# Kernel tuning notes

Measured on AMD Instinct MI355X. Metric: run time of the kernel, lower is better.

The kernel has to match this reference:

```python
import jax, jax.numpy as jnp
import numpy as np
import math

L, B, D, H = 2048, 4, 1024, 16
DK = D // H
DFF = 4 * D
EPS = 1e-5


def setup_inputs() -> dict:
    key = jax.random.key(0)
    ks = jax.random.split(key, 16)
    s = 1.0 / math.sqrt(D)
    sf = 1.0 / math.sqrt(DFF)
    return {
        "x": jax.random.normal(ks[0], (L, B, D), jnp.float32),
        "Wq": jax.random.normal(ks[1], (D, D), jnp.float32) * s,
        "bq": jnp.zeros((D,), jnp.float32),
        "Wk": jax.random.normal(ks[2], (D, D), jnp.float32) * s,
        "bk": jnp.zeros((D,), jnp.float32),
        "Wv": jax.random.normal(ks[3], (D, D), jnp.float32) * s,
        "bv": jnp.zeros((D,), jnp.float32),
        "Wo": jax.random.normal(ks[4], (D, D), jnp.float32) * s,
        "bo": jnp.zeros((D,), jnp.float32),
        "W1": jax.random.normal(ks[5], (D, DFF), jnp.float32) * s,
        "b1": jnp.zeros((DFF,), jnp.float32),
        "W2": jax.random.normal(ks[6], (DFF, D), jnp.float32) * sf,
        "b2": jnp.zeros((D,), jnp.float32),
        "g1": jnp.ones((D,), jnp.float32),
        "be1": jnp.zeros((D,), jnp.float32),
        "g2": jnp.ones((D,), jnp.float32),
        "be2": jnp.zeros((D,), jnp.float32),
    }


def _layer_norm(x, g, b):
    mu = jnp.mean(x, axis=-1, keepdims=True)
    var = jnp.var(x, axis=-1, keepdims=True)
    return (x - mu) * jax.lax.rsqrt(var + EPS) * g + b


def reference(x, Wq, bq, Wk, bk, Wv, bv, Wo, bo, W1, b1, W2, b2, g1, be1, g2, be2):
    # x: (L, B, D)
    q = x @ Wq + bq
    k = x @ Wk + bk
    v = x @ Wv + bv
    # (L,B,H,dk) -> (B,H,L,dk)
    q = q.reshape(L, B, H, DK).transpose(1, 2, 0, 3)
    k = k.reshape(L, B, H, DK).transpose(1, 2, 0, 3)
    v = v.reshape(L, B, H, DK).transpose(1, 2, 0, 3)
    scale = 1.0 / math.sqrt(DK)
    scores = jnp.einsum('bhqd,bhkd->bhqk', q, k) * scale
    w = jax.nn.softmax(scores, axis=-1)
    attn = jnp.einsum('bhqk,bhkd->bhqd', w, v)  # (B,H,L,dk)
    attn = attn.transpose(2, 0, 1, 3).reshape(L, B, D)
    attn_out = attn @ Wo + bo
    x = _layer_norm(x + attn_out, g1, be1)
    h = jax.nn.gelu(x @ W1 + b1, approximate=False)
    ff = h @ W2 + b2
    return _layer_norm(x + ff, g2, be2)
```

## Files before the change

### kernel.cpp

```cpp
#include <hip/hip_runtime.h>

#define L_   2048
#define B_   4
#define D_   1024
#define H_   16
#define DK_  64
#define DFF_ 4096
#define NT_  (L_*B_)

typedef unsigned short u16;
typedef unsigned int   u32;
typedef __bf16 bf16x8 __attribute__((ext_vector_type(8)));
typedef float  f32x4  __attribute__((ext_vector_type(4)));

__device__ __forceinline__ u16 f2bf(float f) {
  u32 u = __float_as_uint(f);
  u += 0x7fffu + ((u >> 16) & 1u);
  return (u16)(u >> 16);
}

#define GLDS16(g, l) __builtin_amdgcn_global_load_lds( \
    (const __attribute__((address_space(1))) void*)(g), \
    (__attribute__((address_space(3))) void*)(l), 16, 0, 0)

__global__ __launch_bounds__(256) void transpose_w_k(
    const float* __restrict__ W, u16* __restrict__ Wt, int K, int N)
{
  __shared__ float tile[32][33];
  int n0 = blockIdx.x * 32, k0 = blockIdx.y * 32;
  int tx = threadIdx.x, ty = threadIdx.y;
#pragma unroll
  for (int i = ty; i < 32; i += 8)
    tile[i][tx] = W[(size_t)(k0 + i) * N + n0 + tx];
  __syncthreads();
#pragma unroll
  for (int i = ty; i < 32; i += 8)
    Wt[(size_t)(n0 + i) * K + k0 + tx] = f2bf(tile[tx][i]);
}

__global__ __launch_bounds__(256) void f32_to_bf16_k(
    const float* __restrict__ in, u16* __restrict__ out, int n4)
{
  int i = blockIdx.x * 256 + threadIdx.x;
  if (i >= n4) return;
  float4 v = ((const float4*)in)[i];
  uint2 r;
  r.x = (u32)f2bf(v.x) | ((u32)f2bf(v.y) << 16);
  r.y = (u32)f2bf(v.z) | ((u32)f2bf(v.w) << 16);
  ((uint2*)out)[i] = r;
}

__global__ __launch_bounds__(256) void bias_concat_k(
    const float* __restrict__ bq, const float* __restrict__ bk,
    const float* __restrict__ bv, float* __restrict__ o)
{
  int i = blockIdx.x * 256 + threadIdx.x;
  float v = (i < 1024) ? bq[i] : ((i < 2048) ? bk[i - 1024] : bv[i - 2048]);
  o[i] = v;
}

template<int BN, int EPI>
__global__ __launch_bounds__(512, 2)
void gemm_pipe(const u16* __restrict__ A, const u16* __restrict__ Bt,
               const float* __restrict__ bias, const float* __restrict__ res,
               u16* __restrict__ outb, float* __restrict__ outf,
               int M, int N, int K)
{
  constexpr int BM = 256;
  constexpr int NI  = 2 + BN / 128;
  constexpr int NWN = BN / 64;
  constexpr int NWM = 8 / NWN;
  constexpr int MIT = (BM / NWM) / 16;
  constexpr int NPH = MIT / 4;
  constexpr int BUFB = (BM + BN) * 64;
  __shared__ char SM[4 * BUFB];

  const int tid = threadIdx.x;
  const int w = tid >> 6, lane = tid & 63;
  const int l15 = lane & 15, l4 = lane >> 4;
  const int NK = K >> 5;

  const int gx = gridDim.x;
  int nwg = gx * gridDim.y;
  int id = blockIdx.y * gx + blockIdx.x;
  int q = nwg >> 3, r = nwg & 7;
  int xcd = id & 7, idx = id >> 3;
  int wg = (xcd < r ? xcd * (q + 1) : r * (q + 1) + (xcd - r) * q) + idx;
  const int m0 = (wg / gx) * BM, n0 = (wg % gx) * BN;
  const int wm = (w / NWN) * (BM / NWM), wn = (w % NWN) * 64;

  const u16* gsrc[NI];
#pragma unroll
  for (int k = 0; k < NI; ++k) {
    int o = k * 8192 + tid * 16;
    int col8 = (o >> 4) & 3;
    if (o < BM * 64) {
      int rrow = o >> 6;
      gsrc[k] = A + (size_t)(m0 + rrow) * K + col8 * 8;
    } else {
      int br = (o - BM * 64) >> 6;
      gsrc[k] = Bt + (size_t)(n0 + br) * K + col8 * 8;
    }
  }

  auto stage = [&](int t3, int k) {
    const u16* s = (t3 < NK) ? gsrc[k] + (size_t)t3 * 32 : gsrc[k];
    GLDS16(s, SM + (t3 & 3) * BUFB + k * 8192 + w * 1024);
  };

  for (int t3 = 0; t3 < 3; ++t3)
#pragma unroll
    for (int k = 0; k < NI; ++k) stage(t3, k);
  if constexpr (BN == 256) asm volatile("s_waitcnt vmcnt(8)" ::: "memory");
  else                     asm volatile("s_waitcnt vmcnt(6)" ::: "memory");
  asm volatile("s_barrier" ::: "memory");

  f32x4 acc[MIT][4];
#pragma unroll
  for (int i = 0; i < MIT; ++i)
#pragma unroll
    for (int j = 0; j < 4; ++j) acc[i][j] = (f32x4){0.f, 0.f, 0.f, 0.f};

  for (int t = 0; t < NK; ++t) {
    const char* rb = SM + (t & 3) * BUFB;
    bf16x8 bfr[4];
#pragma unroll
    for (int ph = 0; ph < NPH; ++ph) {
      bf16x8 af[4];
#pragma unroll
      for (int mi = 0; mi < 4; ++mi)
        af[mi] = *(const bf16x8*)(rb + (wm + ph * 64 + mi * 16 + l15) * 64 + l4 * 16);
      if (ph == 0) {
#pragma unroll
        for (int nj = 0; nj < 4; ++nj)
          bfr[nj] = *(const bf16x8*)(rb + BM * 64 + (wn + nj * 16 + l15) * 64 + l4 * 16);
      }
      if constexpr (NPH == 2) {
        stage(t + 3, ph * 2 + 0);
        stage(t + 3, ph * 2 + 1);
      } else {
        stage(t + 3, 0); stage(t + 3, 1); stage(t + 3, 2);
      }
      asm volatile("s_barrier" ::: "memory");
      __builtin_amdgcn_s_setprio(1);
#pragma unroll
      for (int mi = 0; mi < 4; ++mi)
#pragma unroll
        for (int nj = 0; nj < 4; ++nj)
          acc[ph * 4 + mi][nj] = __builtin_amdgcn_mfma_f32_16x16x32_bf16(
              af[mi], bfr[nj], acc[ph * 4 + mi][nj], 0, 0, 0);
      __builtin_amdgcn_s_setprio(0);
      if (ph == NPH - 1) {
        if constexpr (BN == 256) asm volatile("s_waitcnt vmcnt(8)" ::: "memory");
        else                     asm volatile("s_waitcnt vmcnt(6)" ::: "memory");
      }
      asm volatile("s_barrier" ::: "memory");
    }
  }
  asm volatile("s_waitcnt vmcnt(0)" ::: "memory");

  const int gm = m0 + wm + l4 * 4;
  const int gn = n0 + wn + l15;
#pragma unroll
  for (int mi = 0; mi < MIT; ++mi) {
#pragma unroll
    for (int nj = 0; nj < 4; ++nj) {
      int col = gn + nj * 16;
      float bv = bias[col];
#pragma unroll
      for (int rr = 0; rr < 4; ++rr) {
        int row = gm + mi * 16 + rr;
        float v = acc[mi][nj][rr] + bv;
        if (EPI == 1) {
          size_t idxo = (size_t)row * N + col;
          outf[idxo] = v + res[idxo];
        } else if (EPI == 2) {
          float gv = 0.5f * v * (1.f + erff(v * 0.70710678118654752f));
          outb[(size_t)row * N + col] = f2bf(gv);
        } else {
          int which = col >> 10, c1 = col & 1023;
          int ll = row >> 2, bb = row & 3;
          int hh = c1 >> 6, dd = c1 & 63;
          outb[(size_t)which * (L_ * B_ * D_ / 4) * 4 / 2 * 2 +
               ((((size_t)(bb * H_ + hh)) * L_ + ll) << 6) + dd
               - (size_t)which * 0] = f2bf(v);
        }
      }
    }
  }
}

template<>
__global__ __launch_bounds__(512, 2)
void gemm_pipe<256, 3>(const u16* __restrict__ A, const u16* __restrict__ Bt,
                       const float* __restrict__ bias, const float* __restrict__ res,
                       u16* __restrict__ outb, float* __restrict__ outf,
                       int M, int N, int K)
{
  constexpr int BM = 256, BN = 256;
  constexpr int NI = 4, NWN = 4, NWM = 2, MIT = 8, NPH = 2;
  constexpr int BUFB = (BM + BN) * 64;
  __shared__ char SM[4 * BUFB];

  const int tid = threadIdx.x;
  const int w = tid >> 6, lane = tid & 63;
  const int l15 = lane & 15, l4 = lane >> 4;
  const int NK = K >> 5;

  const int gx = gridDim.x;
  int nwg = gx * gridDim.y;
  int id = blockIdx.y * gx + blockIdx.x;
  int q = nwg >> 3, r = nwg & 7;
  int xcd = id & 7, idx = id >> 3;
  int wg = (xcd < r ? xcd * (q + 1) : r * (q + 1) + (xcd - r) * q) + idx;
  const int m0 = (wg / gx) * BM, n0 = (wg % gx) * BN;
  const int wm = (w / NWN) * (BM / NWM), wn = (w % NWN) * 64;

  const u16* gsrc[NI];
#pragma unroll
  for (int k = 0; k < NI; ++k) {
    int o = k * 8192 + tid * 16;
    int col8 = (o >> 4) & 3;
    if (o < BM * 64) {
      int rrow = o >> 6;
      gsrc[k] = A + (size_t)(m0 + rrow) * K + col8 * 8;
    } else {
      int br = (o - BM * 64) >> 6;
      gsrc[k] = Bt + (size_t)(n0 + br) * K + col8 * 8;
    }
  }

  auto stage = [&](int t3, int k) {
    const u16* s = (t3 < NK) ? gsrc[k] + (size_t)t3 * 32 : gsrc[k];
    GLDS16(s, SM + (t3 & 3) * BUFB + k * 8192 + w * 1024);
  };

  for (int t3 = 0; t3 < 3; ++t3)
#pragma unroll
    for (int k = 0; k < NI; ++k) stage(t3, k);
  asm volatile("s_waitcnt vmcnt(8)" ::: "memory");
  asm volatile("s_barrier" ::: "memory");

  f32x4 acc[MIT][4];
#pragma unroll
  for (int i = 0; i < MIT; ++i)
#pragma unroll
    for (int j = 0; j < 4; ++j) acc[i][j] = (f32x4){0.f, 0.f, 0.f, 0.f};

  for (int t = 0; t < NK; ++t) {
    const char* rb = SM + (t & 3) * BUFB;
    bf16x8 bfr[4];
#pragma unroll
    for (int ph = 0; ph < NPH; ++ph) {
      bf16x8 af[4];
#pragma unroll
      for (int mi = 0; mi < 4; ++mi)
        af[mi] = *(const bf16x8*)(rb + (wm + ph * 64 + mi * 16 + l15) * 64 + l4 * 16);
      if (ph == 0) {
#pragma unroll
        for (int nj = 0; nj < 4; ++nj)
          bfr[nj] = *(const bf16x8*)(rb + BM * 64 + (wn + nj * 16 + l15) * 64 + l4 * 16);
      }
      stage(t + 3, ph * 2 + 0);
      stage(t + 3, ph * 2 + 1);
      asm volatile("s_barrier" ::: "memory");
      __builtin_amdgcn_s_setprio(1);
#pragma unroll
      for (int mi = 0; mi < 4; ++mi)
#pragma unroll
        for (int nj = 0; nj < 4; ++nj)
          acc[ph * 4 + mi][nj] = __builtin_amdgcn_mfma_f32_16x16x32_bf16(
              af[mi], bfr[nj], acc[ph * 4 + mi][nj], 0, 0, 0);
      __builtin_amdgcn_s_setprio(0);
      if (ph == NPH - 1) asm volatile("s_waitcnt vmcnt(8)" ::: "memory");
      asm volatile("s_barrier" ::: "memory");
    }
  }
  asm volatile("s_waitcnt vmcnt(0)" ::: "memory");

  const int gm = m0 + wm + l4 * 4;
  const int gn = n0 + wn + l15;
#pragma unroll
  for (int mi = 0; mi < MIT; ++mi) {
#pragma unroll
    for (int nj = 0; nj < 4; ++nj) {
      int col = gn + nj * 16;
      float bv = bias[col];
#pragma unroll
      for (int rr = 0; rr < 4; ++rr) {
        int row = gm + mi * 16 + rr;
        float v = acc[mi][nj][rr] + bv;
        int which = col >> 10, c1 = col & 1023;
        int ll = row >> 2, bb = row & 3;
        int hh = c1 >> 6, dd = c1 & 63;
        outb[(size_t)which * 8388608 +
             ((((size_t)(bb * H_ + hh)) * L_ + ll) << 6) + dd] = f2bf(v);
      }
    }
  }
}

__global__ __launch_bounds__(256, 4)
void attn_fwd2(const u16* __restrict__ qp, const u16* __restrict__ kp,
               const u16* __restrict__ vp, u16* __restrict__ op)
{
  __shared__ u16 Ks[64 * 64];
  __shared__ u16 Vt[64 * 64];
  const int tid = threadIdx.x, w = tid >> 6, lane = tid & 63;
  const int l15 = lane & 15, l4 = lane >> 4;
  const int n = blockIdx.x;
  const int bh = (n & 7) | ((n >> 8) << 3);
  const int qi = (n >> 3) & 31;
  const int q0 = qi * 64;
  const u16* qb = qp + (size_t)bh * L_ * DK_;
  const u16* kb = kp + (size_t)bh * L_ * DK_;
  const u16* vb = vp + (size_t)bh * L_ * DK_;

  bf16x8 qf[2];
#pragma unroll
  for (int kk = 0; kk < 2; ++kk)
    qf[kk] = *(const bf16x8*)&qb[(size_t)(q0 + w * 16 + l15) * DK_ + kk * 32 + l4 * 8];

  f32x4 accO[4];
#pragma unroll
  for (int i = 0; i < 4; ++i) accO[i] = (f32x4){0.f, 0.f, 0.f, 0.f};
  float mrun = -1e30f, lsum = 0.f;
  const float SC = 0.18033688011112042f;

  int rho0 = tid >> 3, rho1 = (256 + tid) >> 3, c = lane & 7;
  int kv0 = (rho0 & 32) | ((rho0 & 12) << 1) | ((rho0 & 16) >> 2) | (rho0 & 3);
  int kv1 = (rho1 & 32) | ((rho1 & 12) << 1) | ((rho1 & 16) >> 2) | (rho1 & 3);
  const u16* ksrc0 = kb + (size_t)kv0 * DK_ + ((c ^ (rho0 & 7)) << 3);
  const u16* ksrc1 = kb + (size_t)kv1 * DK_ + ((c ^ (rho1 & 7)) << 3);
  u16* kdst0 = &Ks[(w * 64) * 8];
  u16* kdst1 = &Ks[(256 + w * 64) * 8];

  const int vseg = tid & 7, vkvp = tid >> 3;
  const u16* vsrc = vb + (size_t)(vkvp * 2) * DK_ + vseg * 8;
  u32* vdst[8];
#pragma unroll
  for (int dd2 = 0; dd2 < 4; ++dd2) {
    int d0 = vseg * 8 + dd2 * 2, d1 = d0 + 1;
    vdst[dd2 * 2] = (u32*)((char*)Vt + d0 * 128 +
        ((((vkvp >> 2) ^ (d0 & 7) ^ (d0 >> 3)) << 4) | ((vkvp & 3) << 2)));
    vdst[dd2 * 2 + 1] = (u32*)((char*)Vt + d1 * 128 +
        ((((vkvp >> 2) ^ (d1 & 7) ^ (d1 >> 3)) << 4) | ((vkvp & 3) << 2)));
  }

  for (int t0 = 0; t0 < L_; t0 += 64) {
    __syncthreads();
    GLDS16(ksrc0 + (size_t)t0 * DK_, kdst0);
    GLDS16(ksrc1 + (size_t)t0 * DK_, kdst1);
    {
      const u16* src = vsrc + (size_t)t0 * DK_;
      uint4 a = *(const uint4*)src;
      uint4 b = *(const uint4*)(src + DK_);
#pragma unroll
      for (int dd2 = 0; dd2 < 4; ++dd2) {
        u32 ai = ((const u32*)&a)[dd2], bi = ((const u32*)&b)[dd2];
        *vdst[dd2 * 2]     = (ai & 0xFFFFu) | (bi << 16);
        *vdst[dd2 * 2 + 1] = (ai >> 16) | (bi & 0xFFFF0000u);
      }
    }
    __syncthreads();

    f32x4 s[4];
#pragma unroll
    for (int i = 0; i < 4; ++i) s[i] = (f32x4){0.f, 0.f, 0.f, 0.f};
#pragma unroll
    for (int kk = 0; kk < 2; ++kk) {
#pragma unroll
      for (int nb = 0; nb < 4; ++nb) {
        int row = nb * 16 + l15;
        bf16x8 kf = *(const bf16x8*)((const char*)Ks + row * 128 +
                                     (((kk * 4 + l4) ^ (row & 7)) << 4));
        s[nb] = __builtin_amdgcn_mfma_f32_16x16x32_bf16(kf, qf[kk], s[nb], 0, 0, 0);
      }
    }

    float pm = s[0][0];
#pragma unroll
    for (int i = 0; i < 4; ++i)
#pragma unroll
      for (int rr = 0; rr < 4; ++rr) pm = fmaxf(pm, s[i][rr]);
    pm = fmaxf(pm, __shfl_xor(pm, 16));
    pm = fmaxf(pm, __shfl_xor(pm, 32));
    float pmS = pm * SC;
    if (!__all(pmS - mrun <= 8.f)) {
      float mn = fmaxf(mrun, pmS);
      float alpha = exp2f(mrun - mn);
      mrun = mn;
      lsum *= alpha;
#pragma unroll
      for (int rr = 0; rr < 4; ++rr) {
        float a4 = __shfl(alpha, l4 * 4 + rr);
        accO[0][rr] *= a4; accO[1][rr] *= a4; accO[2][rr] *= a4; accO[3][rr] *= a4;
      }
    }
#pragma unroll
    for (int i = 0; i < 4; ++i)
#pragma unroll
      for (int rr = 0; rr < 4; ++rr) s[i][rr] = exp2f(fmaf(s[i][rr], SC, -mrun));
    float ps = 0.f;
#pragma unroll
    for (int i = 0; i < 4; ++i)
      ps += (s[i][0] + s[i][1]) + (s[i][2] + s[i][3]);
    ps += __shfl_xor(ps, 16);
    ps += __shfl_xor(ps, 32);
    lsum += ps;

    u32 pk[2][4];
#pragma unroll
    for (int kk = 0; kk < 2; ++kk)
#pragma unroll
      for (int j2 = 0; j2 < 4; ++j2) {
        int nb = kk * 2 + (j2 >> 1);
        int rr = (j2 & 1) * 2;
        u32 rres;
        asm("v_cvt_pk_bf16_f32 %0, %1, %2" : "=v"(rres) : "v"(s[nb][rr]), "v"(s[nb][rr + 1]));
        pk[kk][j2] = rres;
      }

#pragma unroll
    for (int kk = 0; kk < 2; ++kk) {
      bf16x8 pa;
      ((u32*)&pa)[0] = pk[kk][0];
      ((u32*)&pa)[1] = pk[kk][1];
      ((u32*)&pa)[2] = pk[kk][2];
      ((u32*)&pa)[3] = pk[kk][3];
#pragma unroll
      for (int nb2 = 0; nb2 < 4; ++nb2) {
        int drow = nb2 * 16 + l15;
        bf16x8 vf = *(const bf16x8*)((const char*)Vt + drow * 128 +
                                     (((kk * 4 + l4) ^ (drow & 7) ^ (drow >> 3)) << 4));
        accO[nb2] = __builtin_amdgcn_mfma_f32_16x16x32_bf16(pa, vf, accO[nb2], 0, 0, 0);
      }
    }
  }

  float invl = 1.f / lsum;
  const int bb = bh >> 4, hh = bh & 15;
#pragma unroll
  for (int rr = 0; rr < 4; ++rr) {
    float rl = __shfl(invl, l4 * 4 + rr);
    int qg = q0 + w * 16 + l4 * 4 + rr;
    size_t base = ((size_t)qg * B_ + bb) * D_ + hh * 64;
#pragma unroll
    for (int nb2 = 0; nb2 < 4; ++nb2)
      op[base + nb2 * 16 + l15] = f2bf(accO[nb2][rr] * rl);
  }
}

__global__ __launch_bounds__(256) void layernorm_k(
    const float* __restrict__ y, const float* __restrict__ g, const float* __restrict__ be,
    float* __restrict__ of, u16* __restrict__ ob)
{
  int row = blockIdx.x, tid = threadIdx.x;
  const float4 v = *(const float4*)&y[(size_t)row * D_ + tid * 4];
  float s = v.x + v.y + v.z + v.w;
  float ss = v.x * v.x + v.y * v.y + v.z * v.z + v.w * v.w;
#pragma unroll
  for (int msk = 32; msk >= 1; msk >>= 1) {
    s += __shfl_xor(s, msk);
    ss += __shfl_xor(ss, msk);
  }
  __shared__ float rs[4], rss[4];
  if ((tid & 63) == 0) { rs[tid >> 6] = s; rss[tid >> 6] = ss; }
  __syncthreads();
  s = rs[0] + rs[1] + rs[2] + rs[3];
  ss = rss[0] + rss[1] + rss[2] + rss[3];
  float mu = s * (1.f / D_);
  float var = ss * (1.f / D_) - mu * mu;
  float rstd = rsqrtf(var + 1e-5f);
  int c = tid * 4;
  float4 o;
  o.x = (v.x - mu) * rstd * g[c + 0] + be[c + 0];
  o.y = (v.y - mu) * rstd * g[c + 1] + be[c + 1];
  o.z = (v.z - mu) * rstd * g[c + 2] + be[c + 2];
  o.w = (v.w - mu) * rstd * g[c + 3] + be[c + 3];
  *(float4*)&of[(size_t)row * D_ + c] = o;
  if (ob) {
    uint2 r;
    r.x = (u32)f2bf(o.x) | ((u32)f2bf(o.y) << 16);
    r.y = (u32)f2bf(o.z) | ((u32)f2bf(o.w) << 16);
    *(uint2*)&ob[(size_t)row * D_ + c] = r;
  }
}

extern "C" void kernel_launch(void* const* d_in, const int* in_sizes, int n_in,
                              void* d_out, int out_size, void* d_ws, size_t ws_size,
                              hipStream_t stream)
{
  const float* x   = (const float*)d_in[0];
  const float* Wq  = (const float*)d_in[1];
  const float* bq  = (const float*)d_in[2];
  const float* Wk  = (const float*)d_in[3];
  const float* bk  = (const float*)d_in[4];
  const float* Wv  = (const float*)d_in[5];
  const float* bv  = (const float*)d_in[6];
  const float* Wo  = (const float*)d_in[7];
  const float* bo  = (const float*)d_in[8];
  const float* W1  = (const float*)d_in[9];
  const float* b1  = (const float*)d_in[10];
  const float* W2  = (const float*)d_in[11];
  const float* b2  = (const float*)d_in[12];
  const float* g1  = (const float*)d_in[13];
  const float* be1 = (const float*)d_in[14];
  const float* g2  = (const float*)d_in[15];
  const float* be2 = (const float*)d_in[16];

  char* ws = (char*)d_ws;
  const size_t MB = 1024 * 1024;
  u16* WqT  = (u16*)(ws + 0 * MB);
  u16* WkT  = (u16*)(ws + 2 * MB);
  u16* WvT  = (u16*)(ws + 4 * MB);
  u16* WoT  = (u16*)(ws + 6 * MB);
  u16* W1T  = (u16*)(ws + 8 * MB);
  u16* W2T  = (u16*)(ws + 16 * MB);
  u16* xb   = (u16*)(ws + 24 * MB);
  u16* qp   = (u16*)(ws + 40 * MB);
  u16* astd = (u16*)(ws + 88 * MB);
  float* y1  = (float*)(ws + 104 * MB);
  float* x1f = (float*)(ws + 136 * MB);
  u16*   x1b = (u16*)(ws + 168 * MB);
  float* bcat = (float*)(ws + 184 * MB);
  u16*   hbuf = (u16*)(ws + 40 * MB);
  u16* kp = qp + 8388608;
  u16* vp = qp + 16777216;

  dim3 tb(32, 8);
  transpose_w_k<<<dim3(32, 32), tb, 0, stream>>>(Wq, WqT, D_, D_);
  transpose_w_k<<<dim3(32, 32), tb, 0, stream>>>(Wk, WkT, D_, D_);
  transpose_w_k<<<dim3(32, 32), tb, 0, stream>>>(Wv, WvT, D_, D_);
  transpose_w_k<<<dim3(32, 32), tb, 0, stream>>>(Wo, WoT, D_, D_);
  transpose_w_k<<<dim3(128, 32), tb, 0, stream>>>(W1, W1T, D_, DFF_);
  transpose_w_k<<<dim3(32, 128), tb, 0, stream>>>(W2, W2T, DFF_, D_);
  f32_to_bf16_k<<<NT_ * D_ / 4 / 256, 256, 0, stream>>>(x, xb, NT_ * D_ / 4);
  bias_concat_k<<<12, 256, 0, stream>>>(bq, bk, bv, bcat);

  gemm_pipe<256, 3><<<dim3(12, 32), 512, 0, stream>>>(
      xb, WqT, bcat, nullptr, qp, nullptr, NT_, 3072, D_);

  attn_fwd2<<<2048, 256, 0, stream>>>(qp, kp, vp, astd);

  gemm_pipe<128, 1><<<dim3(8, 32), 512, 0, stream>>>(
      astd, WoT, bo, x, nullptr, y1, NT_, D_, D_);
  layernorm_k<<<NT_, 256, 0, stream>>>(y1, g1, be1, x1f, x1b);
  gemm_pipe<256, 2><<<dim3(16, 32), 512, 0, stream>>>(
      x1b, W1T, b1, nullptr, hbuf, nullptr, NT_, DFF_, D_);
  gemm_pipe<128, 1><<<dim3(8, 32), 512, 0, stream>>>(
      hbuf, W2T, b2, x1f, nullptr, y1, NT_, D_, DFF_);
  layernorm_k<<<NT_, 256, 0, stream>>>(y1, g2, be2, (float*)d_out, nullptr);
}
```

Before: 519.8 us.

## Store residual-path intermediates in bf16, fold softmax scale into Q, merge weight transposes

```diff
diff --git a/kernel.cpp b/kernel.cpp
--- a/kernel.cpp
+++ b/kernel.cpp
@@ -18,11 +18,16 @@
   u += 0x7fffu + ((u >> 16) & 1u);
   return (u16)(u >> 16);
 }
+__device__ __forceinline__ float bf2f(u32 lo16) {
+  return __uint_as_float(lo16 << 16);
+}
 
 #define GLDS16(g, l) __builtin_amdgcn_global_load_lds( \
     (const __attribute__((address_space(1))) void*)(g), \
     (__attribute__((address_space(3))) void*)(l), 16, 0, 0)
 
+#define SCQ_ 0.18033688011112042f
+
 __global__ __launch_bounds__(256) void transpose_w_k(
     const float* __restrict__ W, u16* __restrict__ Wt, int K, int N)
 {
@@ -36,6 +41,26 @@
 #pragma unroll
   for (int i = ty; i < 32; i += 8)
     Wt[(size_t)(n0 + i) * K + k0 + tx] = f2bf(tile[tx][i]);
+}
+
+__global__ __launch_bounds__(256) void transpose_w4_k(
+    const float* __restrict__ W0, const float* __restrict__ W1,
+    const float* __restrict__ W2, const float* __restrict__ W3,
+    u16* __restrict__ dst)
+{
+  __shared__ float tile[32][33];
+  int z = blockIdx.z;
+  const float* W = (z == 0) ? W0 : (z == 1) ? W1 : (z == 2) ? W2 : W3;
+  u16* Wt = dst + (size_t)z * 1048576;
+  int n0 = blockIdx.x * 32, k0 = blockIdx.y * 32;
+  int tx = threadIdx.x, ty = threadIdx.y;
+#pragma unroll
+  for (int i = ty; i < 32; i += 8)
+    tile[i][tx] = W[(size_t)(k0 + i) * 1024 + n0 + tx];
+  __syncthreads();
+#pragma unroll
+  for (int i = ty; i < 32; i += 8)
+    Wt[(size_t)(n0 + i) * 1024 + k0 + tx] = f2bf(tile[tx][i]);
 }
 
 __global__ __launch_bounds__(256) void f32_to_bf16_k(
@@ -62,9 +87,8 @@
 template<int BN, int EPI>
 __global__ __launch_bounds__(512, 2)
 void gemm_pipe(const u16* __restrict__ A, const u16* __restrict__ Bt,
-               const float* __restrict__ bias, const float* __restrict__ res,
-               u16* __restrict__ outb, float* __restrict__ outf,
-               int M, int N, int K)
+               const float* __restrict__ bias, const void* __restrict__ res,
+               u16* __restrict__ outb, int M, int N, int K)
 {
   constexpr int BM = 256;
   constexpr int NI  = 2 + BN / 128;
@@ -171,130 +195,23 @@
       for (int rr = 0; rr < 4; ++rr) {
         int row = gm + mi * 16 + rr;
         float v = acc[mi][nj][rr] + bv;
-        if (EPI == 1) {
-          size_t idxo = (size_t)row * N + col;
-          outf[idxo] = v + res[idxo];
-        } else if (EPI == 2) {
+        if (EPI == 2) {
           float gv = 0.5f * v * (1.f + erff(v * 0.70710678118654752f));
           outb[(size_t)row * N + col] = f2bf(gv);
-        } else {
+        } else if (EPI == 3) {
           int which = col >> 10, c1 = col & 1023;
           int ll = row >> 2, bb = row & 3;
           int hh = c1 >> 6, dd = c1 & 63;
-          outb[(size_t)which * (L_ * B_ * D_ / 4) * 4 / 2 * 2 +
-               ((((size_t)(bb * H_ + hh)) * L_ + ll) << 6) + dd
-               - (size_t)which * 0] = f2bf(v);
+          if (which == 0) v *= SCQ_;
+          outb[(size_t)which * 8388608 +
+               ((((size_t)(bb * H_ + hh)) * L_ + ll) << 6) + dd] = f2bf(v);
+        } else if (EPI == 5) {
+          size_t idxo = (size_t)row * N + col;
+          outb[idxo] = f2bf(v + ((const float*)res)[idxo]);
+        } else {
+          size_t idxo = (size_t)row * N + col;
+          outb[idxo] = f2bf(v + bf2f(((const u16*)res)[idxo]));
         }
-      }
-    }
-  }
-}
-
-template<>
-__global__ __launch_bounds__(512, 2)
-void gemm_pipe<256, 3>(const u16* __restrict__ A, const u16* __restrict__ Bt,
-                       const float* __restrict__ bias, const float* __restrict__ res,
-                       u16* __restrict__ outb, float* __restrict__ outf,
-                       int M, int N, int K)
-{
-  constexpr int BM = 256, BN = 256;
-  constexpr int NI = 4, NWN = 4, NWM = 2, MIT = 8, NPH = 2;
-  constexpr int BUFB = (BM + BN) * 64;
-  __shared__ char SM[4 * BUFB];
-
-  const int tid = threadIdx.x;
-  const int w = tid >> 6, lane = tid & 63;
-  const int l15 = lane & 15, l4 = lane >> 4;
-  const int NK = K >> 5;
-
-  const int gx = gridDim.x;
-  int nwg = gx * gridDim.y;
-  int id = blockIdx.y * gx + blockIdx.x;
-  int q = nwg >> 3, r = nwg & 7;
-  int xcd = id & 7, idx = id >> 3;
-  int wg = (xcd < r ? xcd * (q + 1) : r * (q + 1) + (xcd - r) * q) + idx;
-  const int m0 = (wg / gx) * BM, n0 = (wg % gx) * BN;
-  const int wm = (w / NWN) * (BM / NWM), wn = (w % NWN) * 64;
-
-  const u16* gsrc[NI];
-#pragma unroll
-  for (int k = 0; k < NI; ++k) {
-    int o = k * 8192 + tid * 16;
-    int col8 = (o >> 4) & 3;
-    if (o < BM * 64) {
-      int rrow = o >> 6;
-      gsrc[k] = A + (size_t)(m0 + rrow) * K + col8 * 8;
-    } else {
-      int br = (o - BM * 64) >> 6;
-      gsrc[k] = Bt + (size_t)(n0 + br) * K + col8 * 8;
-    }
-  }
-
-  auto stage = [&](int t3, int k) {
-    const u16* s = (t3 < NK) ? gsrc[k] + (size_t)t3 * 32 : gsrc[k];
-    GLDS16(s, SM + (t3 & 3) * BUFB + k * 8192 + w * 1024);
-  };
-
-  for (int t3 = 0; t3 < 3; ++t3)
-#pragma unroll
-    for (int k = 0; k < NI; ++k) stage(t3, k);
-  asm volatile("s_waitcnt vmcnt(8)" ::: "memory");
-  asm volatile("s_barrier" ::: "memory");
-
-  f32x4 acc[MIT][4];
-#pragma unroll
-  for (int i = 0; i < MIT; ++i)
-#pragma unroll
-    for (int j = 0; j < 4; ++j) acc[i][j] = (f32x4){0.f, 0.f, 0.f, 0.f};
-
-  for (int t = 0; t < NK; ++t) {
-    const char* rb = SM + (t & 3) * BUFB;
-    bf16x8 bfr[4];
-#pragma unroll
-    for (int ph = 0; ph < NPH; ++ph) {
-      bf16x8 af[4];
-#pragma unroll
-      for (int mi = 0; mi < 4; ++mi)
-        af[mi] = *(const bf16x8*)(rb + (wm + ph * 64 + mi * 16 + l15) * 64 + l4 * 16);
-      if (ph == 0) {
-#pragma unroll
-        for (int nj = 0; nj < 4; ++nj)
-          bfr[nj] = *(const bf16x8*)(rb + BM * 64 + (wn + nj * 16 + l15) * 64 + l4 * 16);
-      }
-      stage(t + 3, ph * 2 + 0);
-      stage(t + 3, ph * 2 + 1);
-      asm volatile("s_barrier" ::: "memory");
-      __builtin_amdgcn_s_setprio(1);
-#pragma unroll
-      for (int mi = 0; mi < 4; ++mi)
-#pragma unroll
-        for (int nj = 0; nj < 4; ++nj)
-          acc[ph * 4 + mi][nj] = __builtin_amdgcn_mfma_f32_16x16x32_bf16(
-              af[mi], bfr[nj], acc[ph * 4 + mi][nj], 0, 0, 0);
-      __builtin_amdgcn_s_setprio(0);
-      if (ph == NPH - 1) asm volatile("s_waitcnt vmcnt(8)" ::: "memory");
-      asm volatile("s_barrier" ::: "memory");
-    }
-  }
-  asm volatile("s_waitcnt vmcnt(0)" ::: "memory");
-
-  const int gm = m0 + wm + l4 * 4;
-  const int gn = n0 + wn + l15;
-#pragma unroll
-  for (int mi = 0; mi < MIT; ++mi) {
-#pragma unroll
-    for (int nj = 0; nj < 4; ++nj) {
-      int col = gn + nj * 16;
-      float bv = bias[col];
-#pragma unroll
-      for (int rr = 0; rr < 4; ++rr) {
-        int row = gm + mi * 16 + rr;
-        float v = acc[mi][nj][rr] + bv;
-        int which = col >> 10, c1 = col & 1023;
-        int ll = row >> 2, bb = row & 3;
-        int hh = c1 >> 6, dd = c1 & 63;
-        outb[(size_t)which * 8388608 +
-             ((((size_t)(bb * H_ + hh)) * L_ + ll) << 6) + dd] = f2bf(v);
       }
     }
   }
@@ -325,13 +242,12 @@
 #pragma unroll
   for (int i = 0; i < 4; ++i) accO[i] = (f32x4){0.f, 0.f, 0.f, 0.f};
   float mrun = -1e30f, lsum = 0.f;
-  const float SC = 0.18033688011112042f;
-
-  int rho0 = tid >> 3, rho1 = (256 + tid) >> 3, c = lane & 7;
+
+  int rho0 = tid >> 3, rho1 = (256 + tid) >> 3, cseg = lane & 7;
   int kv0 = (rho0 & 32) | ((rho0 & 12) << 1) | ((rho0 & 16) >> 2) | (rho0 & 3);
   int kv1 = (rho1 & 32) | ((rho1 & 12) << 1) | ((rho1 & 16) >> 2) | (rho1 & 3);
-  const u16* ksrc0 = kb + (size_t)kv0 * DK_ + ((c ^ (rho0 & 7)) << 3);
-  const u16* ksrc1 = kb + (size_t)kv1 * DK_ + ((c ^ (rho1 & 7)) << 3);
+  const u16* ksrc0 = kb + (size_t)kv0 * DK_ + ((cseg ^ (rho0 & 7)) << 3);
+  const u16* ksrc1 = kb + (size_t)kv1 * DK_ + ((cseg ^ (rho1 & 7)) << 3);
   u16* kdst0 = &Ks[(w * 64) * 8];
   u16* kdst1 = &Ks[(256 + w * 64) * 8];
 
@@ -378,16 +294,19 @@
       }
     }
 
-    float pm = s[0][0];
-#pragma unroll
-    for (int i = 0; i < 4; ++i)
-#pragma unroll
-      for (int rr = 0; rr < 4; ++rr) pm = fmaxf(pm, s[i][rr]);
+    float pm = fmaxf(fmaxf(s[0][0], s[0][1]), s[0][2]);
+    pm = fmaxf(fmaxf(pm, s[0][3]), s[1][0]);
+    pm = fmaxf(fmaxf(pm, s[1][1]), s[1][2]);
+    pm = fmaxf(fmaxf(pm, s[1][3]), s[2][0]);
+    pm = fmaxf(fmaxf(pm, s[2][1]), s[2][2]);
+    pm = fmaxf(fmaxf(pm, s[2][3]), s[3][0]);
+    pm = fmaxf(fmaxf(pm, s[3][1]), s[3][2]);
+    pm = fmaxf(pm, s[3][3]);
     pm = fmaxf(pm, __shfl_xor(pm, 16));
     pm = fmaxf(pm, __shfl_xor(pm, 32));
-    float pmS = pm * SC;
-    if (!__all(pmS - mrun <= 8.f)) {
-      float mn = fmaxf(mrun, pmS);
+
+    if (!__all(pm - mrun <= 8.f)) {
+      float mn = fmaxf(mrun, pm);
       float alpha = exp2f(mrun - mn);
       mrun = mn;
       lsum *= alpha;
@@ -400,7 +319,7 @@
 #pragma unroll
     for (int i = 0; i < 4; ++i)
 #pragma unroll
-      for (int rr = 0; rr < 4; ++rr) s[i][rr] = exp2f(fmaf(s[i][rr], SC, -mrun));
+      for (int rr = 0; rr < 4; ++rr) s[i][rr] = exp2f(s[i][rr] - mrun);
     float ps = 0.f;
 #pragma unroll
     for (int i = 0; i < 4; ++i)
@@ -451,14 +370,16 @@
   }
 }
 
-__global__ __launch_bounds__(256) void layernorm_k(
-    const float* __restrict__ y, const float* __restrict__ g, const float* __restrict__ be,
+__global__ __launch_bounds__(256) void layernorm_bf_k(
+    const u16* __restrict__ y, const float* __restrict__ g, const float* __restrict__ be,
     float* __restrict__ of, u16* __restrict__ ob)
 {
   int row = blockIdx.x, tid = threadIdx.x;
-  const float4 v = *(const float4*)&y[(size_t)row * D_ + tid * 4];
-  float s = v.x + v.y + v.z + v.w;
-  float ss = v.x * v.x + v.y * v.y + v.z * v.z + v.w * v.w;
+  uint2 raw = *(const uint2*)&y[(size_t)row * D_ + tid * 4];
+  float v0 = bf2f(raw.x & 0xffffu), v1 = bf2f(raw.x >> 16);
+  float v2 = bf2f(raw.y & 0xffffu), v3 = bf2f(raw.y >> 16);
+  float s = (v0 + v1) + (v2 + v3);
+  float ss = v0 * v0 + v1 * v1 + v2 * v2 + v3 * v3;
 #pragma unroll
   for (int msk = 32; msk >= 1; msk >>= 1) {
     s += __shfl_xor(s, msk);
@@ -473,16 +394,18 @@
   float var = ss * (1.f / D_) - mu * mu;
   float rstd = rsqrtf(var + 1e-5f);
   int c = tid * 4;
-  float4 o;
-  o.x = (v.x - mu) * rstd * g[c + 0] + be[c + 0];
-  o.y = (v.y - mu) * rstd * g[c + 1] + be[c + 1];
-  o.z = (v.z - mu) * rstd * g[c + 2] + be[c + 2];
-  o.w = (v.w - mu) * rstd * g[c + 3] + be[c + 3];
-  *(float4*)&of[(size_t)row * D_ + c] = o;
+  float o0 = (v0 - mu) * rstd * g[c + 0] + be[c + 0];
+  float o1 = (v1 - mu) * rstd * g[c + 1] + be[c + 1];
+  float o2 = (v2 - mu) * rstd * g[c + 2] + be[c + 2];
+  float o3 = (v3 - mu) * rstd * g[c + 3] + be[c + 3];
+  if (of) {
+    float4 o = {o0, o1, o2, o3};
+    *(float4*)&of[(size_t)row * D_ + c] = o;
+  }
   if (ob) {
     uint2 r;
-    r.x = (u32)f2bf(o.x) | ((u32)f2bf(o.y) << 16);
-    r.y = (u32)f2bf(o.z) | ((u32)f2bf(o.w) << 16);
+    r.x = (u32)f2bf(o0) | ((u32)f2bf(o1) << 16);
+    r.y = (u32)f2bf(o2) | ((u32)f2bf(o3) << 16);
     *(uint2*)&ob[(size_t)row * D_ + c] = r;
   }
 }
@@ -500,9 +423,9 @@
   const float* bv  = (const float*)d_in[6];
   const float* Wo  = (const float*)d_in[7];
   const float* bo  = (const float*)d_in[8];
-  const float* W1  = (const float*)d_in[9];
+  const float* W1f = (const float*)d_in[9];
   const float* b1  = (const float*)d_in[10];
-  const float* W2  = (const float*)d_in[11];
+  const float* W2f = (const float*)d_in[11];
   const float* b2  = (const float*)d_in[12];
   const float* g1  = (const float*)d_in[13];
   const float* be1 = (const float*)d_in[14];
@@ -512,43 +435,37 @@
   char* ws = (char*)d_ws;
   const size_t MB = 1024 * 1024;
   u16* WqT  = (u16*)(ws + 0 * MB);
-  u16* WkT  = (u16*)(ws + 2 * MB);
-  u16* WvT  = (u16*)(ws + 4 * MB);
   u16* WoT  = (u16*)(ws + 6 * MB);
   u16* W1T  = (u16*)(ws + 8 * MB);
   u16* W2T  = (u16*)(ws + 16 * MB);
   u16* xb   = (u16*)(ws + 24 * MB);
   u16* qp   = (u16*)(ws + 40 * MB);
   u16* astd = (u16*)(ws + 88 * MB);
-  float* y1  = (float*)(ws + 104 * MB);
-  float* x1f = (float*)(ws + 136 * MB);
-  u16*   x1b = (u16*)(ws + 168 * MB);
-  float* bcat = (float*)(ws + 184 * MB);
-  u16*   hbuf = (u16*)(ws + 40 * MB);
+  u16* yb   = (u16*)(ws + 104 * MB);
+  u16* x1b  = (u16*)(ws + 120 * MB);
+  u16* hbuf = (u16*)(ws + 136 * MB);
+  float* bcat = (float*)(ws + 200 * MB);
   u16* kp = qp + 8388608;
   u16* vp = qp + 16777216;
 
   dim3 tb(32, 8);
-  transpose_w_k<<<dim3(32, 32), tb, 0, stream>>>(Wq, WqT, D_, D_);
-  transpose_w_k<<<dim3(32, 32), tb, 0, stream>>>(Wk, WkT, D_, D_);
-  transpose_w_k<<<dim3(32, 32), tb, 0, stream>>>(Wv, WvT, D_, D_);
-  transpose_w_k<<<dim3(32, 32), tb, 0, stream>>>(Wo, WoT, D_, D_);
-  transpose_w_k<<<dim3(128, 32), tb, 0, stream>>>(W1, W1T, D_, DFF_);
-  transpose_w_k<<<dim3(32, 128), tb, 0, stream>>>(W2, W2T, DFF_, D_);
+  transpose_w4_k<<<dim3(32, 32, 4), tb, 0, stream>>>(Wq, Wk, Wv, Wo, WqT);
+  transpose_w_k<<<dim3(128, 32), tb, 0, stream>>>(W1f, W1T, D_, DFF_);
+  transpose_w_k<<<dim3(32, 128), tb, 0, stream>>>(W2f, W2T, DFF_, D_);
   f32_to_bf16_k<<<NT_ * D_ / 4 / 256, 256, 0, stream>>>(x, xb, NT_ * D_ / 4);
   bias_concat_k<<<12, 256, 0, stream>>>(bq, bk, bv, bcat);
 
-  gemm_pipe<256, 3><<<dim3(12, 32), 512, 0, stream>>>(
-      xb, WqT, bcat, nullptr, qp, nullptr, NT_, 3072, D_);
+  gemm_pipe<128, 3><<<dim3(24, 32), 512, 0, stream>>>(
+      xb, WqT, bcat, nullptr, qp, NT_, 3072, D_);
 
   attn_fwd2<<<2048, 256, 0, stream>>>(qp, kp, vp, astd);
 
-  gemm_pipe<128, 1><<<dim3(8, 32), 512, 0, stream>>>(
-      astd, WoT, bo, x, nullptr, y1, NT_, D_, D_);
-  layernorm_k<<<NT_, 256, 0, stream>>>(y1, g1, be1, x1f, x1b);
+  gemm_pipe<128, 5><<<dim3(8, 32), 512, 0, stream>>>(
+      astd, WoT, bo, x, yb, NT_, D_, D_);
+  layernorm_bf_k<<<NT_, 256, 0, stream>>>(yb, g1, be1, nullptr, x1b);
   gemm_pipe<256, 2><<<dim3(16, 32), 512, 0, stream>>>(
-      x1b, W1T, b1, nullptr, hbuf, nullptr, NT_, DFF_, D_);
-  gemm_pipe<128, 1><<<dim3(8, 32), 512, 0, stream>>>(
-      hbuf, W2T, b2, x1f, nullptr, y1, NT_, D_, DFF_);
-  layernorm_k<<<NT_, 256, 0, stream>>>(y1, g2, be2, (float*)d_out, nullptr);
-}
+      x1b, W1T, b1, nullptr, hbuf, NT_, DFF_, D_);
+  gemm_pipe<128, 6><<<dim3(8, 32), 512, 0, stream>>>(
+      hbuf, W2T, b2, x1b, yb, NT_, D_, DFF_);
+  layernorm_bf_k<<<NT_, 256, 0, stream>>>(yb, g2, be2, (float*)d_out, nullptr);
+}
```

Measured after the change: 500.0 us. 3.8% less time.
